# Optimization experiments

Measured on AMD Instinct MI355X. Metric: run time of the kernel, lower is better.

Reference implementation:

```python
import jax, jax.numpy as jnp
import numpy as np

B, S, E, HID, NTR, NCAL, CW, VOCAB, POS = 4096, 201, 32, 512, 4, 8, 16, 32, 256
LN_EPS = 1e-5


def _ln(x, g, b):
    m = x.mean(-1, keepdims=True)
    v = ((x - m) ** 2).mean(-1, keepdims=True)
    return (x - m) * jax.lax.rsqrt(v + LN_EPS) * g + b


def setup_inputs() -> dict:
    key = jax.random.key(0)
    ks = jax.random.split(key, 24)
    g = lambda i, shape, s=0.1: (jax.random.normal(ks[i], shape, jnp.float32) * s)
    return dict(
        encoded_seq=jax.random.randint(ks[0], (B, S), 0, VOCAB, jnp.int32),
        experiment_id=jax.random.randint(ks[1], (B,), 0, NCAL, jnp.int32),
        tok_emb=g(2, (VOCAB, E), 1.0),
        pos_emb=g(3, (POS, E), 1.0),
        ln1_g=jnp.ones((NTR, E)), ln1_b=jnp.zeros((NTR, E)),
        wq=g(4, (NTR, E, E)), wk=g(5, (NTR, E, E)), wv=g(6, (NTR, E, E)),
        bq=g(7, (NTR, E), 0.01), bk=g(8, (NTR, E), 0.01), bv=g(9, (NTR, E), 0.01),
        wo=g(10, (NTR, E, E)), bo=g(11, (NTR, E), 0.01),
        ln2_g=jnp.ones((NTR, E)), ln2_b=jnp.zeros((NTR, E)),
        w1=g(12, (NTR, E, HID)), b1=g(13, (NTR, HID), 0.01),
        w2=g(14, (NTR, HID, E)), b2=g(15, (NTR, E), 0.01),
        lnf_g=jnp.ones((E,)), lnf_b=jnp.zeros((E,)),
        wpen=g(16, (E, 1)), bpen=g(17, (1,), 0.01),
        wfan=g(18, (1, CW)), bfan=g(19, (CW,), 0.01),
        wcal=g(20, (NCAL, CW, 1)), bcal=g(21, (NCAL, 1), 0.01),
    )


def reference(encoded_seq, experiment_id, tok_emb, pos_emb,
              ln1_g, ln1_b, wq, wk, wv, bq, bk, bv, wo, bo,
              ln2_g, ln2_b, w1, b1, w2, b2,
              lnf_g, lnf_b, wpen, bpen, wfan, bfan, wcal, bcal):
    # embedding + positional add: [B,S,E]
    x = tok_emb[encoded_seq] + pos_emb[jnp.arange(S)]
    scale = 1.0 / jnp.sqrt(jnp.float32(E))  # num_heads=1 => head_dim=E
    for i in range(NTR):
        n = _ln(x, ln1_g[i], ln1_b[i])
        q = n @ wq[i] + bq[i]
        k = n @ wk[i] + bk[i]
        v = n @ wv[i] + bv[i]
        a = jax.nn.softmax(jnp.einsum('bqe,bke->bqk', q, k) * scale, axis=-1)
        att = jnp.einsum('bqk,bke->bqe', a, v) @ wo[i] + bo[i]
        x = x + att
        h = _ln(x, ln2_g[i], ln2_b[i])
        x = x + (jax.nn.silu(h @ w1[i] + b1[i]) @ w2[i] + b2[i])
    contrib = _ln(x, lnf_g, lnf_b) @ wpen + bpen        # [B,S,1]
    underlying = contrib.sum(axis=-2)                    # [B,1]
    pre = jax.nn.elu(underlying @ wfan + bfan)           # [B,CW]
    # all calibrator heads at once: [B,NCAL]
    all_corr = jnp.einsum('bc,ncj->bn', pre, wcal) + bcal[:, 0]
    mask = jax.nn.one_hot(experiment_id, NCAL, dtype=pre.dtype)  # exactly the (exp==id) mask-sum
    corrected = (all_corr * mask).sum(-1, keepdims=True) + underlying
    return corrected.squeeze()
```

## Files before the change

kernel.cpp:

```cpp
#include <hip/hip_runtime.h>


#define SS   201
#define SP   208
#define NMT  13
#define EE   32
#define HIDN 512
#define NTRL 4
#define CWN  16
#define BB   4096
#define K2ST 20
#define VWST 216

#define VW2_OFF  16640
#define SMEM_SZ  30464

#define WS_FRAG  0
#define WS_BIAS  294912
#define WS_B1    299008
#define WS_FIN   307200
#define L2E      1.4426950408889634f
#define QCE      0.2550546813f

typedef unsigned short u16;
typedef unsigned int   u32;
typedef short bf16x4 __attribute__((ext_vector_type(4)));
typedef short bf16x8 __attribute__((ext_vector_type(8)));
typedef float f32x4  __attribute__((ext_vector_type(4)));
typedef float f32x2  __attribute__((ext_vector_type(2)));
typedef unsigned int u32x4 __attribute__((ext_vector_type(4)));

__device__ __forceinline__ f32x4 MF(bf16x8 a, bf16x8 b, f32x4 c){
  return __builtin_amdgcn_mfma_f32_16x16x32_bf16(a, b, c, 0, 0, 0);
}
__device__ __forceinline__ float bf2f(u16 u){ return __uint_as_float(((u32)u)<<16); }
__device__ __forceinline__ u16 f2bf(float f){
  u32 u = __float_as_uint(f);
  u += 0x7fffu + ((u>>16)&1u);
  return (u16)(u>>16);
}
__device__ __forceinline__ u32 pk2bf(f32x2 v){
#if defined(__has_builtin) && __has_builtin(__builtin_amdgcn_cvt_pk_bf16_f32)
  auto r = __builtin_amdgcn_cvt_pk_bf16_f32(v.x, v.y);
  u32 u; __builtin_memcpy(&u, &r, 4); return u;
#else
  return ((__float_as_uint(v.x)+0x8000u)>>16) | ((__float_as_uint(v.y)+0x8000u) & 0xffff0000u);
#endif
}
__device__ __forceinline__ f32x2 upk2(u32 d){
  return f32x2{ __uint_as_float(d<<16), __uint_as_float(d & 0xffff0000u) };
}
template<bool F32>
__device__ __forceinline__ float ldv(const void* p, int i){
  if (F32) return ((const float*)p)[i];
  return bf2f(((const u16*)p)[i]);
}
template<bool F32>
__device__ __forceinline__ u16 ldbf(const void* p, int i){
  if (F32) return f2bf(((const float*)p)[i]);
  return ((const u16*)p)[i];
}
__device__ __forceinline__ bf16x8 cat44(bf16x4 lo, bf16x4 hi){
  bf16x8 r = {lo[0],lo[1],lo[2],lo[3],hi[0],hi[1],hi[2],hi[3]};
  return r;
}
__device__ __forceinline__ bf16x8 mk8(u32 a0, u32 a1, u32 a2, u32 a3){
  u32 t[4] = {a0,a1,a2,a3};
  bf16x8 r; __builtin_memcpy(&r, t, 16); return r;
}
__device__ __forceinline__ u32 spk(f32x2 z){
  const f32x2 nl2e2 = {-L2E, -L2E};
  const f32x2 one2  = {1.f, 1.f};
  f32x2 a = z * nl2e2;
  f32x2 e = { __builtin_amdgcn_exp2f(a.x), __builtin_amdgcn_exp2f(a.y) };
  f32x2 d = one2 + e;
  f32x2 rc = { __builtin_amdgcn_rcpf(d.x), __builtin_amdgcn_rcpf(d.y) };
  f32x2 s = z * rc;
  return pk2bf(s);
}

__device__ __forceinline__ int sniff_bf16(const void* tok_emb, int tid){
  int sane = 0;
  if (tid < 64){
    u16 wd = ((const u16*)tok_emb)[tid];
    int e = (wd >> 7) & 0xFF;
    sane = (e >= 100 && e <= 140) ? 1 : 0;
  }
  return (__syncthreads_count(sane) >= 52) ? 1 : 0;
}

template<bool F32>
__device__ __forceinline__ void frag_body(const void* wq, const void* wk,
    const void* wv, const void* wo, const void* w1, const void* w2, void* ws)
{
  int t = blockIdx.x;
  int l = t / 72, k = t % 72;
  int lane = threadIdx.x, l16 = lane & 15, quad = lane >> 4;
  bf16x8 v;
  if (k < 8){
    int mat = k >> 1, half = k & 1;
    if (mat == 2){
      int col = half*16 + l16;
      #pragma unroll
      for (int j=0;j<8;j++){
        int pr = quad*4 + (j&3) + ((j&4)<<2);
        float acc = 0.f;
        for (int e=0;e<EE;e++)
          acc += ldv<F32>(wv, l*1024 + pr*32 + e) * ldv<F32>(wo, l*1024 + e*32 + col);
        v[j] = (short)f2bf(acc);
      }
    } else if (mat == 0){
      #pragma unroll
      for (int j=0;j<8;j++){
        int pr = quad*4 + (j&3) + ((j&4)<<2);
        v[j] = (short)f2bf(QCE * ldv<F32>(wq, l*1024 + pr*32 + half*16 + l16));
      }
    } else {
      const void* src = (mat==1)? wk : wo;
      #pragma unroll
      for (int j=0;j<8;j++){
        int pr = quad*4 + (j&3) + ((j&4)<<2);
        v[j] = (short)ldbf<F32>(src, l*1024 + pr*32 + half*16 + l16);
      }
    }
  } else if (k < 40){
    int nt = k - 8;
    #pragma unroll
    for (int j=0;j<8;j++){
      int pr = quad*4 + (j&3) + ((j&4)<<2);
      v[j] = (short)ldbf<F32>(w1, l*16384 + pr*512 + nt*16 + l16);
    }
  } else {
    int kc = (k-40)>>1, nh = (k-40)&1;
    #pragma unroll
    for (int j=0;j<8;j++){
      int hh = kc*32 + ((j&4) ? 16 : 0) + quad*4 + (j&3);
      v[j] = (short)ldbf<F32>(w2, l*16384 + hh*32 + nh*16 + l16);
    }
  }
  *(bf16x8*)((char*)ws + WS_FRAG + t*1024 + lane*16) = v;
}

__global__ __launch_bounds__(64) void fmt_frags(
    const void* __restrict__ tok_emb,
    const void* __restrict__ wq, const void* __restrict__ wk,
    const void* __restrict__ wv, const void* __restrict__ wo,
    const void* __restrict__ w1, const void* __restrict__ w2,
    void* __restrict__ ws)
{
  if (sniff_bf16(tok_emb, threadIdx.x)) frag_body<false>(wq,wk,wv,wo,w1,w2,ws);
  else                                  frag_body<true >(wq,wk,wv,wo,w1,w2,ws);
}

template<bool F32>
__device__ __forceinline__ void bias_body(
    const void* bq, const void* bk, const void* bv, const void* wo, const void* bo,
    const void* ln1_g, const void* ln1_b, const void* ln2_g, const void* ln2_b,
    const void* b1, const void* b2,
    const void* lnf_g, const void* lnf_b, const void* wpen, const void* bpen,
    const void* wfan, const void* bfan, const void* wcal, const void* bcal,
    void* ws)
{
  int tid = threadIdx.x, idx = tid & 31, grp = tid >> 5;
  float* BW  = (float*)((char*)ws + WS_BIAS);
  float* BW1 = (float*)((char*)ws + WS_B1);
  float* FW  = (float*)((char*)ws + WS_FIN);
  for (int l=0;l<NTRL;l++){
    float v = 0.f;
    switch(grp){
      case 0: v = QCE * ldv<F32>(bq, l*32+idx); break;
      case 1: v = ldv<F32>(bk, l*32+idx); break;
      case 2: {
        float acc = ldv<F32>(bo, l*32+idx);
        for (int e=0;e<EE;e++) acc += ldv<F32>(bv, l*32+e) * ldv<F32>(wo, l*1024 + e*32 + idx);
        v = acc; break;
      }
      case 3: v = ldv<F32>(ln1_g, l*32+idx); break;
      case 4: v = ldv<F32>(ln1_b, l*32+idx); break;
      case 5: v = ldv<F32>(ln2_g, l*32+idx); break;
      case 6: v = ldv<F32>(ln2_b, l*32+idx); break;
      case 7: v = ldv<F32>(b2,   l*32+idx); break;
    }
    BW[l*256 + tid] = v;
  }
  for (int i=tid; i<NTRL*HIDN; i+=256) BW1[i] = ldv<F32>(b1, i);
  if (tid < 32){
    FW[tid]    = ldv<F32>(lnf_g, tid);
    FW[32+tid] = ldv<F32>(lnf_b, tid);
    FW[64+tid] = ldv<F32>(wpen, tid);
  }
  if (tid == 0) FW[96] = ldv<F32>(bpen, 0);
  if (tid < 16){ FW[97+tid] = ldv<F32>(wfan, tid); FW[113+tid] = ldv<F32>(bfan, tid); }
  if (tid < 128) FW[129+tid] = ldv<F32>(wcal, tid);
  if (tid < 8)   FW[257+tid] = ldv<F32>(bcal, tid);
}

__global__ __launch_bounds__(256) void fmt_bias(
    const void* __restrict__ tok_emb,
    const void* __restrict__ bq, const void* __restrict__ bk,
    const void* __restrict__ bv, const void* __restrict__ wo, const void* __restrict__ bo,
    const void* __restrict__ ln1_g, const void* __restrict__ ln1_b,
    const void* __restrict__ ln2_g, const void* __restrict__ ln2_b,
    const void* __restrict__ b1, const void* __restrict__ b2,
    const void* __restrict__ lnf_g, const void* __restrict__ lnf_b,
    const void* __restrict__ wpen, const void* __restrict__ bpen,
    const void* __restrict__ wfan, const void* __restrict__ bfan,
    const void* __restrict__ wcal, const void* __restrict__ bcal,
    void* __restrict__ ws)
{
  if (sniff_bf16(tok_emb, threadIdx.x))
    bias_body<false>(bq,bk,bv,wo,bo,ln1_g,ln1_b,ln2_g,ln2_b,b1,b2,
                     lnf_g,lnf_b,wpen,bpen,wfan,bfan,wcal,bcal,ws);
  else
    bias_body<true >(bq,bk,bv,wo,bo,ln1_g,ln1_b,ln2_g,ln2_b,b1,b2,
                     lnf_g,lnf_b,wpen,bpen,wfan,bfan,wcal,bcal,ws);
}

__device__ __forceinline__ bf16x8 nfrag_x(u32x4 x, float m, float rs,
                                          f32x4 ga, f32x4 gb, f32x4 ba, f32x4 bb){
  f32x2 m2 = {m, m}, rs2 = {rs, rs};
  u32 o0 = pk2bf((upk2(x[0]) - m2) * rs2 * f32x2{ga[0],ga[1]} + f32x2{ba[0],ba[1]});
  u32 o1 = pk2bf((upk2(x[1]) - m2) * rs2 * f32x2{ga[2],ga[3]} + f32x2{ba[2],ba[3]});
  u32 o2 = pk2bf((upk2(x[2]) - m2) * rs2 * f32x2{gb[0],gb[1]} + f32x2{bb[0],bb[1]});
  u32 o3 = pk2bf((upk2(x[3]) - m2) * rs2 * f32x2{gb[2],gb[3]} + f32x2{bb[2],bb[3]});
  return mk8(o0, o1, o2, o3);
}

__device__ __forceinline__ void red_stats(float ps, float pq, float& m, float& rs){
  ps += __shfl_xor(ps, 16); ps += __shfl_xor(ps, 32);
  pq += __shfl_xor(pq, 16); pq += __shfl_xor(pq, 32);
  m  = ps * (1.f/EE);
  rs = rsqrtf(pq * (1.f/EE) - m*m + 1e-5f);
}

template<bool F32>
__device__ __forceinline__ void tr_body(
    const int* seq, const int* expid,
    const void* tok_emb, const void* pos_emb,
    const void* ws, void* out, unsigned char* smem)
{
  u32* K2  = (u32*)smem;
  u16* VW2 = (u16*)(smem + VW2_OFF);

  const int tid  = threadIdx.x;
  const int lane = tid & 63, w = tid >> 6;
  const int l16  = lane & 15, quad = lane >> 4;
  const int b    = blockIdx.x;
  const f32x4 Z  = {0.f,0.f,0.f,0.f};

  u32x4 xp[4];
  float m1[4], rs1[4], m2v[4], rs2v[4];
  {
    const int* srow = seq + b*SS;
    #pragma unroll
    for (int t=0;t<4;t++){
      int m = w + 4*t;
      if (m < NMT){
        int row = m*16 + l16;
        if (row < SS){
          int tok = srow[row];
          #pragma unroll
          for (int p=0;p<4;p++){
            int c = (p<2) ? (quad*4 + 2*p) : (16 + quad*4 + 2*(p-2));
            f32x2 v = { ldv<F32>(tok_emb, tok*EE + c)   + ldv<F32>(pos_emb, row*EE + c),
                        ldv<F32>(tok_emb, tok*EE + c+1) + ldv<F32>(pos_emb, row*EE + c+1) };
            xp[t][p] = pk2bf(v);
          }
        } else {
          xp[t] = u32x4{0u,0u,0u,0u};
        }
        f32x2 s2 = {0.f,0.f}, q2 = {0.f,0.f};
        #pragma unroll
        for (int p=0;p<4;p++){ f32x2 x = upk2(xp[t][p]); s2 += x; q2 += x*x; }
        red_stats(s2.x+s2.y, q2.x+q2.y, m1[t], rs1[t]);
      }
    }
  }

  for (int l = 0; l < NTRL; ++l){
    const char* wsl = (const char*)ws + WS_FRAG + l*73728;
    const float* BW = (const float*)((const char*)ws + WS_BIAS) + l*256;
    bf16x8 bwq0 = *(const bf16x8*)(wsl + 0*1024 + lane*16);
    bf16x8 bwq1 = *(const bf16x8*)(wsl + 1*1024 + lane*16);
    bf16x8 bwk0 = *(const bf16x8*)(wsl + 2*1024 + lane*16);
    bf16x8 bwk1 = *(const bf16x8*)(wsl + 3*1024 + lane*16);
    bf16x8 bwv0 = *(const bf16x8*)(wsl + 4*1024 + lane*16);
    bf16x8 bwv1 = *(const bf16x8*)(wsl + 5*1024 + lane*16);

    bf16x8 aq[4];
    {
      f32x4 ga = *(const f32x4*)(BW + 96 + quad*4);
      f32x4 gb = *(const f32x4*)(BW + 112 + quad*4);
      f32x4 ba = *(const f32x4*)(BW + 128 + quad*4);
      f32x4 bb = *(const f32x4*)(BW + 144 + quad*4);
      f32x4 bq0 = *(const f32x4*)(BW + quad*4);
      f32x4 bq1 = *(const f32x4*)(BW + 16 + quad*4);
      float bk0s = BW[32+l16], bk1s = BW[48+l16];
      f32x4 kc0 = {bk0s,bk0s,bk0s,bk0s};
      f32x4 kc1 = {bk1s,bk1s,bk1s,bk1s};
      #pragma unroll
      for (int t=0;t<4;t++){
        int m = w + 4*t;
        if (m < NMT){
          int m16 = m*16;
          bf16x8 an = nfrag_x(xp[t], m1[t], rs1[t], ga, gb, ba, bb);
          f32x4 ck0 = MF(an, bwk0, kc0), ck1 = MF(an, bwk1, kc1);
          #pragma unroll
          for (int r=0;r<4;r++)
            K2[(m16 + quad*4 + r)*K2ST + l16] = pk2bf(f32x2{ck0[r], ck1[r]});
          f32x4 cw0 = MF(an, bwv0, Z), cw1 = MF(an, bwv1, Z);
          {
            int base = (m == 12) ? (192 + quad*4)
                                 : ((m>>1)*32 + quad*8 + (m&1)*4);
            u32* p0 = (u32*)(VW2 + l16*VWST + base);
            u32* p1 = (u32*)(VW2 + (16+l16)*VWST + base);
            p0[0] = pk2bf(f32x2{cw0[0], cw0[1]});
            p0[1] = pk2bf(f32x2{cw0[2], cw0[3]});
            p1[0] = pk2bf(f32x2{cw1[0], cw1[1]});
            p1[1] = pk2bf(f32x2{cw1[2], cw1[3]});
          }
          f32x4 cq0 = MF(bwq0, an, bq0), cq1 = MF(bwq1, an, bq1);
          aq[t] = mk8(pk2bf(f32x2{cq0[0],cq1[0]}), pk2bf(f32x2{cq0[1],cq1[1]}),
                      pk2bf(f32x2{cq0[2],cq1[2]}), pk2bf(f32x2{cq0[3],cq1[3]}));
        }
      }
    }
    __syncthreads();

    {
      const u16* vb0 = VW2 + l16*VWST;
      const u16* vb1 = VW2 + (16+l16)*VWST;
      f32x4 ob0 = *(const f32x4*)(BW + 64 + quad*4);
      f32x4 ob1 = *(const f32x4*)(BW + 80 + quad*4);
      #pragma unroll
      for (int t=0;t<4;t++){
        int m = w + 4*t;
        if (m < NMT){
          u32 pbw[7][4];
          f32x2 pacc = {0.f, 0.f};
          #pragma unroll
          for (int c=0;c<6;c++){
            const bf16x8 ka = *(const bf16x8*)(K2 + ((2*c  )*16+l16)*K2ST + quad*4);
            const bf16x8 kb = *(const bf16x8*)(K2 + ((2*c+1)*16+l16)*K2ST + quad*4);
            f32x4 S0 = MF(ka, aq[t], Z);
            f32x4 S1 = MF(kb, aq[t], Z);
            f32x2 ea0 = { __builtin_amdgcn_exp2f(S0[0]), __builtin_amdgcn_exp2f(S0[1]) };
            f32x2 eb0 = { __builtin_amdgcn_exp2f(S0[2]), __builtin_amdgcn_exp2f(S0[3]) };
            f32x2 ea1 = { __builtin_amdgcn_exp2f(S1[0]), __builtin_amdgcn_exp2f(S1[1]) };
            f32x2 eb1 = { __builtin_amdgcn_exp2f(S1[2]), __builtin_amdgcn_exp2f(S1[3]) };
            pacc += (ea0 + eb0) + (ea1 + eb1);
            pbw[c][0] = pk2bf(ea0);
            pbw[c][1] = pk2bf(eb0);
            pbw[c][2] = pk2bf(ea1);
            pbw[c][3] = pk2bf(eb1);
          }
          {
            const bf16x8 ka = *(const bf16x8*)(K2 + (12*16+l16)*K2ST + quad*4);
            f32x4 S0 = MF(ka, aq[t], Z);
            f32x2 ea0 = { __builtin_amdgcn_exp2f(S0[0]), __builtin_amdgcn_exp2f(S0[1]) };
            f32x2 eb0 = { __builtin_amdgcn_exp2f(S0[2]), __builtin_amdgcn_exp2f(S0[3]) };
            int kb_ = quad*4;
            if (kb_+0 >= 9) ea0.x = 0.f;
            if (kb_+1 >= 9) ea0.y = 0.f;
            if (kb_+2 >= 9) eb0.x = 0.f;
            if (kb_+3 >= 9) eb0.y = 0.f;
            pacc += ea0 + eb0;
            pbw[6][0] = pk2bf(ea0);
            pbw[6][1] = pk2bf(eb0);
            pbw[6][2] = 0u;
            pbw[6][3] = 0u;
          }
          float part = pacc.x + pacc.y;
          part += __shfl_xor(part, 16);
          part += __shfl_xor(part, 32);
          float inv = __builtin_amdgcn_rcpf(part);

          f32x4 o0 = Z, o1 = Z;
          #pragma unroll
          for (int c=0;c<6;c++){
            bf16x8 A0 = *(const bf16x8*)(vb0 + c*32 + quad*8);
            bf16x8 A1 = *(const bf16x8*)(vb1 + c*32 + quad*8);
            bf16x8 B8 = mk8(pbw[c][0], pbw[c][1], pbw[c][2], pbw[c][3]);
            o0 = MF(A0, B8, o0);
            o1 = MF(A1, B8, o1);
          }
          {
            bf16x4 a0 = *(const bf16x4*)(vb0 + 192 + quad*4);
            bf16x4 a1 = *(const bf16x4*)(vb1 + 192 + quad*4);
            bf16x8 B8 = mk8(pbw[6][0], pbw[6][1], 0u, 0u);
            o0 = MF(cat44(a0, a0), B8, o0);
            o1 = MF(cat44(a1, a1), B8, o1);
          }

          f32x2 r01 = f32x2{o0[0],o0[1]} * inv + (upk2(xp[t][0]) + f32x2{ob0[0],ob0[1]});
          f32x2 r23 = f32x2{o0[2],o0[3]} * inv + (upk2(xp[t][1]) + f32x2{ob0[2],ob0[3]});
          f32x2 s01 = f32x2{o1[0],o1[1]} * inv + (upk2(xp[t][2]) + f32x2{ob1[0],ob1[1]});
          f32x2 s23 = f32x2{o1[2],o1[3]} * inv + (upk2(xp[t][3]) + f32x2{ob1[2],ob1[3]});
          xp[t][0] = pk2bf(r01);
          xp[t][1] = pk2bf(r23);
          xp[t][2] = pk2bf(s01);
          xp[t][3] = pk2bf(s23);
          f32x2 ss = (r01 + r23) + (s01 + s23);
          f32x2 qq = r01*r01; qq += r23*r23; qq += s01*s01; qq += s23*s23;
          red_stats(ss.x+ss.y, qq.x+qq.y, m2v[t], rs2v[t]);
        }
      }
    }
    __syncthreads();

    {
      f32x4 ga = *(const f32x4*)(BW + 160 + quad*4);
      f32x4 gb = *(const f32x4*)(BW + 176 + quad*4);
      f32x4 ba = *(const f32x4*)(BW + 192 + quad*4);
      f32x4 bb = *(const f32x4*)(BW + 208 + quad*4);
      bf16x8 anc[4];
      #pragma unroll
      for (int t=0;t<4;t++){
        int m = w + 4*t;
        if (m < NMT) anc[t] = nfrag_x(xp[t], m2v[t], rs2v[t], ga, gb, ba, bb);
      }
      f32x4 oacc[4][2];
      #pragma unroll
      for (int t=0;t<4;t++){ oacc[t][0] = Z; oacc[t][1] = Z; }
      const char* w1f = wsl + 8*1024;
      const char* w2f = wsl + 40*1024;
      const float* BW1 = (const float*)((const char*)ws + WS_B1) + l*HIDN;

      for (int hp = 0; hp < 16; ++hp){
        bf16x8 a1lo = *(const bf16x8*)(w1f + (2*hp  )*1024 + lane*16);
        bf16x8 a1hi = *(const bf16x8*)(w1f + (2*hp+1)*1024 + lane*16);
        bf16x8 a2e0 = *(const bf16x8*)(w2f + (hp*2  )*1024 + lane*16);
        bf16x8 a2e1 = *(const bf16x8*)(w2f + (hp*2+1)*1024 + lane*16);
        f32x4 b1q0 = *(const f32x4*)(BW1 + hp*32      + quad*4);
        f32x4 b1q1 = *(const f32x4*)(BW1 + hp*32 + 16 + quad*4);
        #pragma unroll
        for (int t=0;t<4;t++){
          int m = w + 4*t;
          if (m < NMT){
            f32x4 z0 = MF(a1lo, anc[t], b1q0);
            f32x4 z1 = MF(a1hi, anc[t], b1q1);
            bf16x8 H8 = mk8(spk(f32x2{z0[0], z0[1]}), spk(f32x2{z0[2], z0[3]}),
                            spk(f32x2{z1[0], z1[1]}), spk(f32x2{z1[2], z1[3]}));
            oacc[t][0] = MF(a2e0, H8, oacc[t][0]);
            oacc[t][1] = MF(a2e1, H8, oacc[t][1]);
          }
        }
      }

      f32x4 b2q0 = *(const f32x4*)(BW + 224 + quad*4);
      f32x4 b2q1 = *(const f32x4*)(BW + 240 + quad*4);
      #pragma unroll
      for (int t=0;t<4;t++){
        int m = w + 4*t;
        if (m < NMT){
          f32x2 r01 = f32x2{oacc[t][0][0], oacc[t][0][1]} + (upk2(xp[t][0]) + f32x2{b2q0[0], b2q0[1]});
          f32x2 r23 = f32x2{oacc[t][0][2], oacc[t][0][3]} + (upk2(xp[t][1]) + f32x2{b2q0[2], b2q0[3]});
          f32x2 s01 = f32x2{oacc[t][1][0], oacc[t][1][1]} + (upk2(xp[t][2]) + f32x2{b2q1[0], b2q1[1]});
          f32x2 s23 = f32x2{oacc[t][1][2], oacc[t][1][3]} + (upk2(xp[t][3]) + f32x2{b2q1[2], b2q1[3]});
          xp[t][0] = pk2bf(r01);
          xp[t][1] = pk2bf(r23);
          xp[t][2] = pk2bf(s01);
          xp[t][3] = pk2bf(s23);
          f32x2 ss = (r01 + r23) + (s01 + s23);
          f32x2 qq = r01*r01; qq += r23*r23; qq += s01*s01; qq += s23*s23;
          red_stats(ss.x+ss.y, qq.x+qq.y, m1[t], rs1[t]);
        }
      }
    }
  }

  const float* FW = (const float*)((const char*)ws + WS_FIN);
  float* HB = (float*)(smem + VW2_OFF);
  if (tid < 32){
    HB[tid]    = FW[tid];
    HB[32+tid] = FW[32+tid];
    HB[64+tid] = FW[64+tid];
  }
  u32* hd = (u32*)smem;
  #pragma unroll
  for (int t=0;t<4;t++){
    int m = w + 4*t;
    if (m < NMT){
      u32* hr = hd + (m*16 + l16)*18;
      hr[quad*2]     = xp[t][0];
      hr[quad*2+1]   = xp[t][1];
      hr[8+quad*2]   = xp[t][2];
      hr[8+quad*2+1] = xp[t][3];
    }
  }
  __syncthreads();
  float part = 0.f;
  if (tid < SS){
    const u32* row = hd + tid*18;
    f32x2 v[16]; f32x2 s2 = {0.f,0.f};
    #pragma unroll
    for (int i=0;i<16;i++){ f32x2 p = upk2(row[i]); v[i] = p; s2 += p; }
    float m = (s2.x+s2.y) * (1.f/EE);
    f32x2 m2 = {m,m};
    f32x2 var2 = {0.f,0.f};
    #pragma unroll
    for (int i=0;i<16;i++){ f32x2 d = v[i]-m2; var2 += d*d; }
    float rs = rsqrtf((var2.x+var2.y)*(1.f/EE) + 1e-5f);
    f32x2 rs2 = {rs, rs};
    f32x2 dot2 = {0.f,0.f};
    #pragma unroll
    for (int i=0;i<16;i++){
      f32x2 g  = {HB[2*i], HB[2*i+1]};
      f32x2 bb = {HB[32+2*i], HB[33+2*i]};
      f32x2 wp = {HB[64+2*i], HB[65+2*i]};
      dot2 += ((v[i]-m2)*rs2*g + bb) * wp;
    }
    part = dot2.x + dot2.y + FW[96];
  }
  #pragma unroll
  for (int off=32; off; off>>=1) part += __shfl_xor(part, off);
  float* REDF = (float*)(smem + VW2_OFF + 512);
  __syncthreads();
  if (lane == 0) REDF[w] = part;
  __syncthreads();
  if (tid == 0){
    float u = REDF[0] + REDF[1] + REDF[2] + REDF[3];
    int ex = expid[b];
    float corr = FW[257+ex];
    #pragma unroll
    for (int c = 0; c < CWN; ++c){
      float pre = u * FW[97+c] + FW[113+c];
      pre = pre > 0.f ? pre : (__expf(pre) - 1.f);
      corr += pre * FW[129 + ex*CWN + c];
    }
    float res = corr + u;
    if (F32) ((float*)out)[b] = res;
    else     ((u16*)out)[b]  = f2bf(res);
  }
}

__global__ __launch_bounds__(256, 3) void tr_kernel(
    const int* __restrict__ seq, const int* __restrict__ expid,
    const void* __restrict__ tok_emb, const void* __restrict__ pos_emb,
    const void* __restrict__ ws, void* __restrict__ out)
{
  __shared__ __align__(16) unsigned char smem[SMEM_SZ];
  if (sniff_bf16(tok_emb, threadIdx.x))
    tr_body<false>(seq, expid, tok_emb, pos_emb, ws, out, smem);
  else
    tr_body<true >(seq, expid, tok_emb, pos_emb, ws, out, smem);
}

extern "C" void kernel_launch(void* const* d_in, const int* in_sizes, int n_in,
                              void* d_out, int out_size, void* d_ws, size_t ws_size,
                              hipStream_t stream)
{
  (void)in_sizes; (void)n_in; (void)ws_size; (void)out_size;
  const void* tok_emb = d_in[2];
  fmt_frags<<<dim3(288), dim3(64), 0, stream>>>(
      tok_emb, d_in[6], d_in[7], d_in[8], d_in[12], d_in[16], d_in[18], d_ws);
  fmt_bias<<<dim3(1), dim3(256), 0, stream>>>(
      tok_emb, d_in[9], d_in[10], d_in[11], d_in[12], d_in[13],
      d_in[4], d_in[5], d_in[14], d_in[15], d_in[17], d_in[19],
      d_in[20], d_in[21], d_in[22], d_in[23],
      d_in[24], d_in[25], d_in[26], d_in[27], d_ws);
  tr_kernel<<<dim3(BB), dim3(256), 0, stream>>>(
      (const int*)d_in[0], (const int*)d_in[1], tok_emb, d_in[3], d_ws, d_out);
}
```

Before: 858.5 us.

## Fold LayerNorm gamma/beta into projection weights and prefetch FFN fragments

LayerNorm scale is folded into the Q/K/V and W1 weight fragments, and the shift is folded into the projection biases at preprocessing time. The per-row normalization in the main kernel then only subtracts the mean and scales by the inverse std, which drops the gamma/beta loads and the extra multiply-adds. The FFN loop also software-prefetches the next iteration's W1/W2 fragments and b1 bias into registers to hide load latency. The cost is higher register pressure from the prefetch buffers, a slightly different bf16 rounding of the folded weights, and a heavier single-block bias preprocessing kernel.

```diff
diff --git a/kernel.cpp b/kernel.cpp
--- a/kernel.cpp
+++ b/kernel.cpp
@@ -55,11 +55,6 @@
   if (F32) return ((const float*)p)[i];
   return bf2f(((const u16*)p)[i]);
 }
-template<bool F32>
-__device__ __forceinline__ u16 ldbf(const void* p, int i){
-  if (F32) return f2bf(((const float*)p)[i]);
-  return ((const u16*)p)[i];
-}
 __device__ __forceinline__ bf16x8 cat44(bf16x4 lo, bf16x4 hi){
   bf16x8 r = {lo[0],lo[1],lo[2],lo[3],hi[0],hi[1],hi[2],hi[3]};
   return r;
@@ -91,7 +86,8 @@
 
 template<bool F32>
 __device__ __forceinline__ void frag_body(const void* wq, const void* wk,
-    const void* wv, const void* wo, const void* w1, const void* w2, void* ws)
+    const void* wv, const void* wo, const void* w1, const void* w2,
+    const void* ln1_g, const void* ln2_g, void* ws)
 {
   int t = blockIdx.x;
   int l = t / 72, k = t % 72;
@@ -107,20 +103,22 @@
         float acc = 0.f;
         for (int e=0;e<EE;e++)
           acc += ldv<F32>(wv, l*1024 + pr*32 + e) * ldv<F32>(wo, l*1024 + e*32 + col);
-        v[j] = (short)f2bf(acc);
+        v[j] = (short)f2bf(acc * ldv<F32>(ln1_g, l*32 + pr));
       }
     } else if (mat == 0){
       #pragma unroll
       for (int j=0;j<8;j++){
         int pr = quad*4 + (j&3) + ((j&4)<<2);
-        v[j] = (short)f2bf(QCE * ldv<F32>(wq, l*1024 + pr*32 + half*16 + l16));
+        float g = ldv<F32>(ln1_g, l*32 + pr);
+        v[j] = (short)f2bf(QCE * g * ldv<F32>(wq, l*1024 + pr*32 + half*16 + l16));
       }
     } else {
       const void* src = (mat==1)? wk : wo;
       #pragma unroll
       for (int j=0;j<8;j++){
         int pr = quad*4 + (j&3) + ((j&4)<<2);
-        v[j] = (short)ldbf<F32>(src, l*1024 + pr*32 + half*16 + l16);
+        float g = (mat==1) ? ldv<F32>(ln1_g, l*32 + pr) : 1.f;
+        v[j] = (short)f2bf(g * ldv<F32>(src, l*1024 + pr*32 + half*16 + l16));
       }
     }
   } else if (k < 40){
@@ -128,14 +126,16 @@
     #pragma unroll
     for (int j=0;j<8;j++){
       int pr = quad*4 + (j&3) + ((j&4)<<2);
-      v[j] = (short)ldbf<F32>(w1, l*16384 + pr*512 + nt*16 + l16);
+      float g = ldv<F32>(ln2_g, l*32 + pr);
+      v[j] = (short)f2bf(g * ldv<F32>(w1, l*16384 + pr*512 + nt*16 + l16));
     }
   } else {
     int kc = (k-40)>>1, nh = (k-40)&1;
     #pragma unroll
     for (int j=0;j<8;j++){
       int hh = kc*32 + ((j&4) ? 16 : 0) + quad*4 + (j&3);
-      v[j] = (short)ldbf<F32>(w2, l*16384 + hh*32 + nh*16 + l16);
+      float wv2 = ldv<F32>(w2, l*16384 + hh*32 + nh*16 + l16);
+      v[j] = (short)f2bf(wv2);
     }
   }
   *(bf16x8*)((char*)ws + WS_FRAG + t*1024 + lane*16) = v;
@@ -146,16 +146,18 @@
     const void* __restrict__ wq, const void* __restrict__ wk,
     const void* __restrict__ wv, const void* __restrict__ wo,
     const void* __restrict__ w1, const void* __restrict__ w2,
+    const void* __restrict__ ln1_g, const void* __restrict__ ln2_g,
     void* __restrict__ ws)
 {
-  if (sniff_bf16(tok_emb, threadIdx.x)) frag_body<false>(wq,wk,wv,wo,w1,w2,ws);
-  else                                  frag_body<true >(wq,wk,wv,wo,w1,w2,ws);
+  if (sniff_bf16(tok_emb, threadIdx.x)) frag_body<false>(wq,wk,wv,wo,w1,w2,ln1_g,ln2_g,ws);
+  else                                  frag_body<true >(wq,wk,wv,wo,w1,w2,ln1_g,ln2_g,ws);
 }
 
 template<bool F32>
 __device__ __forceinline__ void bias_body(
     const void* bq, const void* bk, const void* bv, const void* wo, const void* bo,
-    const void* ln1_g, const void* ln1_b, const void* ln2_g, const void* ln2_b,
+    const void* ln1_b, const void* ln2_b,
+    const void* wq, const void* wk, const void* wv, const void* w1,
     const void* b1, const void* b2,
     const void* lnf_g, const void* lnf_b, const void* wpen, const void* bpen,
     const void* wfan, const void* bfan, const void* wcal, const void* bcal,
@@ -168,22 +170,36 @@
   for (int l=0;l<NTRL;l++){
     float v = 0.f;
     switch(grp){
-      case 0: v = QCE * ldv<F32>(bq, l*32+idx); break;
-      case 1: v = ldv<F32>(bk, l*32+idx); break;
+      case 0: {
+        float acc = ldv<F32>(bq, l*32+idx);
+        for (int e=0;e<EE;e++) acc += ldv<F32>(ln1_b, l*32+e) * ldv<F32>(wq, l*1024 + e*32 + idx);
+        v = QCE * acc; break;
+      }
+      case 1: {
+        float acc = ldv<F32>(bk, l*32+idx);
+        for (int e=0;e<EE;e++) acc += ldv<F32>(ln1_b, l*32+e) * ldv<F32>(wk, l*1024 + e*32 + idx);
+        v = acc; break;
+      }
       case 2: {
         float acc = ldv<F32>(bo, l*32+idx);
-        for (int e=0;e<EE;e++) acc += ldv<F32>(bv, l*32+e) * ldv<F32>(wo, l*1024 + e*32 + idx);
+        for (int f=0;f<EE;f++){
+          float bvv = ldv<F32>(bv, l*32+f);
+          for (int e=0;e<EE;e++) bvv += ldv<F32>(ln1_b, l*32+e) * ldv<F32>(wv, l*1024 + e*32 + f);
+          acc += bvv * ldv<F32>(wo, l*1024 + f*32 + idx);
+        }
         v = acc; break;
       }
-      case 3: v = ldv<F32>(ln1_g, l*32+idx); break;
-      case 4: v = ldv<F32>(ln1_b, l*32+idx); break;
-      case 5: v = ldv<F32>(ln2_g, l*32+idx); break;
-      case 6: v = ldv<F32>(ln2_b, l*32+idx); break;
-      case 7: v = ldv<F32>(b2,   l*32+idx); break;
+      case 7: v = ldv<F32>(b2, l*32+idx); break;
+      default: v = 0.f; break;
     }
     BW[l*256 + tid] = v;
   }
-  for (int i=tid; i<NTRL*HIDN; i+=256) BW1[i] = ldv<F32>(b1, i);
+  for (int i=tid; i<NTRL*HIDN; i+=256){
+    int l = i / HIDN, h = i % HIDN;
+    float acc = ldv<F32>(b1, i);
+    for (int e=0;e<EE;e++) acc += ldv<F32>(ln2_b, l*32+e) * ldv<F32>(w1, l*16384 + e*512 + h);
+    BW1[i] = acc;
+  }
   if (tid < 32){
     FW[tid]    = ldv<F32>(lnf_g, tid);
     FW[32+tid] = ldv<F32>(lnf_b, tid);
@@ -199,8 +215,9 @@
     const void* __restrict__ tok_emb,
     const void* __restrict__ bq, const void* __restrict__ bk,
     const void* __restrict__ bv, const void* __restrict__ wo, const void* __restrict__ bo,
-    const void* __restrict__ ln1_g, const void* __restrict__ ln1_b,
-    const void* __restrict__ ln2_g, const void* __restrict__ ln2_b,
+    const void* __restrict__ ln1_b, const void* __restrict__ ln2_b,
+    const void* __restrict__ wq, const void* __restrict__ wk,
+    const void* __restrict__ wv, const void* __restrict__ w1,
     const void* __restrict__ b1, const void* __restrict__ b2,
     const void* __restrict__ lnf_g, const void* __restrict__ lnf_b,
     const void* __restrict__ wpen, const void* __restrict__ bpen,
@@ -209,20 +226,19 @@
     void* __restrict__ ws)
 {
   if (sniff_bf16(tok_emb, threadIdx.x))
-    bias_body<false>(bq,bk,bv,wo,bo,ln1_g,ln1_b,ln2_g,ln2_b,b1,b2,
+    bias_body<false>(bq,bk,bv,wo,bo,ln1_b,ln2_b,wq,wk,wv,w1,b1,b2,
                      lnf_g,lnf_b,wpen,bpen,wfan,bfan,wcal,bcal,ws);
   else
-    bias_body<true >(bq,bk,bv,wo,bo,ln1_g,ln1_b,ln2_g,ln2_b,b1,b2,
+    bias_body<true >(bq,bk,bv,wo,bo,ln1_b,ln2_b,wq,wk,wv,w1,b1,b2,
                      lnf_g,lnf_b,wpen,bpen,wfan,bfan,wcal,bcal,ws);
 }
 
-__device__ __forceinline__ bf16x8 nfrag_x(u32x4 x, float m, float rs,
-                                          f32x4 ga, f32x4 gb, f32x4 ba, f32x4 bb){
+__device__ __forceinline__ bf16x8 nfrag_x(u32x4 x, float m, float rs){
   f32x2 m2 = {m, m}, rs2 = {rs, rs};
-  u32 o0 = pk2bf((upk2(x[0]) - m2) * rs2 * f32x2{ga[0],ga[1]} + f32x2{ba[0],ba[1]});
-  u32 o1 = pk2bf((upk2(x[1]) - m2) * rs2 * f32x2{ga[2],ga[3]} + f32x2{ba[2],ba[3]});
-  u32 o2 = pk2bf((upk2(x[2]) - m2) * rs2 * f32x2{gb[0],gb[1]} + f32x2{bb[0],bb[1]});
-  u32 o3 = pk2bf((upk2(x[3]) - m2) * rs2 * f32x2{gb[2],gb[3]} + f32x2{bb[2],bb[3]});
+  u32 o0 = pk2bf((upk2(x[0]) - m2) * rs2);
+  u32 o1 = pk2bf((upk2(x[1]) - m2) * rs2);
+  u32 o2 = pk2bf((upk2(x[2]) - m2) * rs2);
+  u32 o3 = pk2bf((upk2(x[3]) - m2) * rs2);
   return mk8(o0, o1, o2, o3);
 }
 
@@ -289,10 +305,6 @@
 
     bf16x8 aq[4];
     {
-      f32x4 ga = *(const f32x4*)(BW + 96 + quad*4);
-      f32x4 gb = *(const f32x4*)(BW + 112 + quad*4);
-      f32x4 ba = *(const f32x4*)(BW + 128 + quad*4);
-      f32x4 bb = *(const f32x4*)(BW + 144 + quad*4);
       f32x4 bq0 = *(const f32x4*)(BW + quad*4);
       f32x4 bq1 = *(const f32x4*)(BW + 16 + quad*4);
       float bk0s = BW[32+l16], bk1s = BW[48+l16];
@@ -303,7 +315,7 @@
         int m = w + 4*t;
         if (m < NMT){
           int m16 = m*16;
-          bf16x8 an = nfrag_x(xp[t], m1[t], rs1[t], ga, gb, ba, bb);
+          bf16x8 an = nfrag_x(xp[t], m1[t], rs1[t]);
           f32x4 ck0 = MF(an, bwk0, kc0), ck1 = MF(an, bwk1, kc1);
           #pragma unroll
           for (int r=0;r<4;r++)
@@ -409,15 +421,11 @@
     __syncthreads();
 
     {
-      f32x4 ga = *(const f32x4*)(BW + 160 + quad*4);
-      f32x4 gb = *(const f32x4*)(BW + 176 + quad*4);
-      f32x4 ba = *(const f32x4*)(BW + 192 + quad*4);
-      f32x4 bb = *(const f32x4*)(BW + 208 + quad*4);
       bf16x8 anc[4];
       #pragma unroll
       for (int t=0;t<4;t++){
         int m = w + 4*t;
-        if (m < NMT) anc[t] = nfrag_x(xp[t], m2v[t], rs2v[t], ga, gb, ba, bb);
+        if (m < NMT) anc[t] = nfrag_x(xp[t], m2v[t], rs2v[t]);
       }
       f32x4 oacc[4][2];
       #pragma unroll
@@ -426,13 +434,24 @@
       const char* w2f = wsl + 40*1024;
       const float* BW1 = (const float*)((const char*)ws + WS_B1) + l*HIDN;
 
+      bf16x8 n1lo = *(const bf16x8*)(w1f + 0*1024 + lane*16);
+      bf16x8 n1hi = *(const bf16x8*)(w1f + 1*1024 + lane*16);
+      bf16x8 n2e0 = *(const bf16x8*)(w2f + 0*1024 + lane*16);
+      bf16x8 n2e1 = *(const bf16x8*)(w2f + 1*1024 + lane*16);
+      f32x4 nb0 = *(const f32x4*)(BW1 + quad*4);
+      f32x4 nb1 = *(const f32x4*)(BW1 + 16 + quad*4);
+
       for (int hp = 0; hp < 16; ++hp){
-        bf16x8 a1lo = *(const bf16x8*)(w1f + (2*hp  )*1024 + lane*16);
-        bf16x8 a1hi = *(const bf16x8*)(w1f + (2*hp+1)*1024 + lane*16);
-        bf16x8 a2e0 = *(const bf16x8*)(w2f + (hp*2  )*1024 + lane*16);
-        bf16x8 a2e1 = *(const bf16x8*)(w2f + (hp*2+1)*1024 + lane*16);
-        f32x4 b1q0 = *(const f32x4*)(BW1 + hp*32      + quad*4);
-        f32x4 b1q1 = *(const f32x4*)(BW1 + hp*32 + 16 + quad*4);
+        bf16x8 a1lo = n1lo, a1hi = n1hi, a2e0 = n2e0, a2e1 = n2e1;
+        f32x4 b1q0 = nb0, b1q1 = nb1;
+        if (hp < 15){
+          n1lo = *(const bf16x8*)(w1f + (2*hp+2)*1024 + lane*16);
+          n1hi = *(const bf16x8*)(w1f + (2*hp+3)*1024 + lane*16);
+          n2e0 = *(const bf16x8*)(w2f + (hp*2+2)*1024 + lane*16);
+          n2e1 = *(const bf16x8*)(w2f + (hp*2+3)*1024 + lane*16);
+          nb0 = *(const f32x4*)(BW1 + (hp+1)*32      + quad*4);
+          nb1 = *(const f32x4*)(BW1 + (hp+1)*32 + 16 + quad*4);
+        }
         #pragma unroll
         for (int t=0;t<4;t++){
           int m = w + 4*t;
@@ -553,10 +572,13 @@
   (void)in_sizes; (void)n_in; (void)ws_size; (void)out_size;
   const void* tok_emb = d_in[2];
   fmt_frags<<<dim3(288), dim3(64), 0, stream>>>(
-      tok_emb, d_in[6], d_in[7], d_in[8], d_in[12], d_in[16], d_in[18], d_ws);
+      tok_emb, d_in[6], d_in[7], d_in[8], d_in[12], d_in[16], d_in[18],
+      d_in[4], d_in[14], d_ws);
   fmt_bias<<<dim3(1), dim3(256), 0, stream>>>(
       tok_emb, d_in[9], d_in[10], d_in[11], d_in[12], d_in[13],
-      d_in[4], d_in[5], d_in[14], d_in[15], d_in[17], d_in[19],
+      d_in[5], d_in[15],
+      d_in[6], d_in[7], d_in[8], d_in[16],
+      d_in[17], d_in[19],
       d_in[20], d_in[21], d_in[22], d_in[23],
       d_in[24], d_in[25], d_in[26], d_in[27], d_ws);
   tr_kernel<<<dim3(BB), dim3(256), 0, stream>>>(
```

After: 948.4 us. +10.5%, slower.
